# Kernel optimization log

Measured on AMD Instinct MI355X. Metric: run time of the kernel, lower is better.

## Reference

```python
import jax, jax.numpy as jnp
import numpy as np

D = 256          # config.entity_dim
DQ = 256         # query feature dim
G = 512          # number of neighbor groups (len(num_neighbors))
PER = 128
N = G * PER      # total candidate entities
CH = [256, 512, 512, 256]  # TCN channel list [D, 2D, 2D, D]
K = 3            # TCN kernel size
HID = 512        # policy net hidden dim


def _p(key, shape):
    return jax.random.normal(key, shape, dtype=jnp.float32) * 0.02


def setup_inputs() -> dict:
    key = jax.random.key(0)
    ks = jax.random.split(key, 32)
    inp = {}
    inp["NEs"] = jax.random.normal(ks[0], (N, D), dtype=jnp.float32)
    inp["nodes"] = jax.random.normal(ks[1], (G, D), dtype=jnp.float32)
    inp["query"] = jax.random.normal(ks[2], (G, DQ), dtype=jnp.float32)
    inp["num_neighbors"] = jnp.full((G,), PER, dtype=jnp.int32)
    inp["action_index"] = jax.random.randint(ks[3], (G,), 0, PER, dtype=jnp.int32)
    # action encoder (linear + relu)
    inp["Wa"] = _p(ks[4], (D, D))
    inp["ba"] = jnp.zeros((D,), jnp.float32)
    # TCN: 4 dilated causal conv levels, 1x1 downsample where channels change
    cin, i = D, 5
    for l, cout in enumerate(CH):
        inp[f"Wc{l}"] = _p(ks[i], (cout, cin, K)); i += 1
        inp[f"bc{l}"] = jnp.zeros((cout,), jnp.float32)
        if cout != cin:
            inp[f"Wd{l}"] = _p(ks[i], (cout, cin)); i += 1
        cin = cout
    # policy net MLP over [state_HS_per_candidate ; hat]
    inp["Wp1"] = _p(ks[i], (DQ + 2 * D + D, HID))
    inp["bp1"] = jnp.zeros((HID,), jnp.float32)
    inp["Wp2"] = _p(ks[i + 1], (HID, 1))
    inp["bp2"] = jnp.zeros((1,), jnp.float32)
    return inp


def _causal_conv(x, w, b, dil):
    # x: [1, C_in, L], w: [C_out, C_in, K] -> causal (left-padded) dilated conv
    k = w.shape[-1]
    y = jax.lax.conv_general_dilated(
        x, w, window_strides=(1,), padding=[((k - 1) * dil, 0)],
        rhs_dilation=(dil,), dimension_numbers=("NCH", "OIH", "NCH"))
    return y + b[None, :, None]


def _tcn(x, params):
    for (w, b, wd), dil in zip(params, (1, 2, 4, 8)):
        y = jax.nn.relu(_causal_conv(x, w, b, dil))
        res = x if wd is None else jnp.einsum("oi,bil->bol", wd, x)
        x = jax.nn.relu(y + res)
    return x


def reference(NEs, nodes, query, num_neighbors, action_index, Wa, ba,
              Wc0, bc0, Wc1, bc1, Wd1, Wc2, bc2, Wc3, bc3, Wd3,
              Wp1, bp1, Wp2, bp2):
    counts = np.asarray(num_neighbors)            # static ragged segment sizes
    g = counts.shape[0]
    seg = jnp.asarray(np.repeat(np.arange(g), counts))
    offsets = np.concatenate([[0], np.cumsum(counts)[:-1]])
    act = np.asarray(action_index)

    hats = jax.nn.relu(NEs @ Wa + ba)                         # [N, D]
    # _Max per group = column-wise max over each ragged segment
    HAts = jax.ops.segment_max(hats, seg, num_segments=g)     # [G, D]
    # chosen-action row per group (last group contributes no hat/node in the loop)
    hats_sel = hats[jnp.asarray(offsets[: g - 1] + act[: g - 1])]  # [G-1, D]

    # state_seq rows: (node_i, HAt_i, hat_i) for i < G-1, then nodes[-1]
    body = jnp.stack([nodes[: g - 1], HAts[: g - 1], hats_sel], axis=1)
    body = body.reshape(3 * (g - 1), -1)
    state_seq = jnp.concatenate([body, nodes[-1:]], axis=0)   # [L, D], L = 3(G-1)+1

    x = state_seq.T[None]                                     # [1, D, L]
    x = _tcn(x, [(Wc0, bc0, None), (Wc1, bc1, Wd1), (Wc2, bc2, None), (Wc3, bc3, Wd3)])
    hs = x[0].T[np.arange(g) * 3]                             # gather node positions -> [G, D]

    state_HS = jnp.concatenate([query, hs, HAts], axis=1)     # [G, DQ + 2D]
    rep = jnp.repeat(state_HS, jnp.asarray(counts), axis=0)   # [N, DQ + 2D]
    h = jax.nn.relu(jnp.concatenate([rep, hats], axis=1) @ Wp1 + bp1)
    Qsa = h @ Wp2 + bp2                                       # [N, 1]
    return Qsa
```

## Files before the change

kernel.cpp:

```cpp
#include <hip/hip_runtime.h>
#include <hip/hip_bf16.h>

#define D 256
#define G 512
#define PER 128
#define NROW (G*PER)
#define LSEQ 1534
#define LP 1536
#define HID 512

typedef __hip_bfloat16 bf16;
typedef __attribute__((ext_vector_type(8))) short bf16x8;
typedef __attribute__((ext_vector_type(4))) float f32x4;


__global__ __launch_bounds__(256) void k_prep(
    const float* __restrict__ Wa, bf16* __restrict__ WAhi, bf16* __restrict__ WAlo,
    const float* __restrict__ Wp1, bf16* __restrict__ WBt,
    bf16* __restrict__ WB1hi, bf16* __restrict__ WB1lo) {
  const int b = blockIdx.x, tid = threadIdx.x;
  if (b < 256) {
    int id = b * 256 + tid;
    int k = id >> 8, n = id & 255;
    float v = Wa[(size_t)k * D + n];
    bf16 h = __float2bfloat16(v);
    bf16 l = __float2bfloat16(v - __bfloat162float(h));
    int dst = (n >> 7) * 32768
            + (((((n >> 4) & 7) * 8 + (k >> 5)) * 64 + ((k >> 3) & 3) * 16 + (n & 15)) * 8)
            + (k & 7);
    WAhi[dst] = h;
    WAlo[dst] = l;
  } else if (b < 768) {
    int id = (b - 256) * 256 + tid;
    int k = id >> 9, n = id & 511;
    float v = Wp1[(size_t)(768 + k) * HID + n];
    int dst = (n >> 7) * 32768
            + (((((n >> 4) & 7) * 8 + (k >> 5)) * 64 + ((k >> 3) & 3) * 16 + (n & 15)) * 8)
            + (k & 7);
    WBt[dst] = __float2bfloat16(v);
  } else {
    int id = (b - 768) * 256 + tid;
    int k = id >> 9, n = id & 511;
    float v = Wp1[(size_t)k * HID + n];
    bf16 h = __float2bfloat16(v);
    bf16 l = __float2bfloat16(v - __bfloat162float(h));
    int kc = k >> 8, kr = k & 255;
    int nc = n >> 7, nr = n & 127;
    int dst = (nc*3 + kc) * 32768
            + ((((nr >> 4) * 8 + (kr >> 5)) * 64 + ((kr >> 3) & 3) * 16 + (nr & 15)) * 8)
            + (kr & 7);
    WB1hi[dst] = h;
    WB1lo[dst] = l;
  }
}

__global__ __launch_bounds__(256, 2) void k_hats_mfma(
    const float* __restrict__ NEs, const bf16* __restrict__ WAhi,
    const bf16* __restrict__ WAlo, const float* __restrict__ ba,
    bf16* __restrict__ hats, float* __restrict__ HAts) {
  __shared__ __align__(16) unsigned short bs[32768];
  __shared__ float wsmax[8][128];

  const int tid = threadIdx.x;
  const int wave = tid >> 6, lane = tid & 63;
  const int ln = lane & 15, quad = lane >> 4;
  const int row0 = blockIdx.x * 128;
  const int g = blockIdx.x;

  bf16x8 afH[2][8], afL[2][8];
  #pragma unroll
  for (int t = 0; t < 2; ++t) {
    const float4* ap = (const float4*)(NEs + (size_t)(row0 + (t*4 + wave)*16 + ln) * D);
    #pragma unroll
    for (int kt = 0; kt < 8; ++kt) {
      float4 x0 = ap[kt*8 + quad*2];
      float4 x1 = ap[kt*8 + quad*2 + 1];
      float xv[8] = {x0.x, x0.y, x0.z, x0.w, x1.x, x1.y, x1.z, x1.w};
      bf16x8 hv, lv;
      #pragma unroll
      for (int e = 0; e < 8; ++e) {
        bf16 h = __float2bfloat16(xv[e]);
        bf16 l = __float2bfloat16(xv[e] - __bfloat162float(h));
        hv[e] = *(short*)&h;
        lv[e] = *(short*)&l;
      }
      afH[t][kt] = hv;
      afL[t][kt] = lv;
    }
  }

  float* bsf = (float*)bs;

  for (int chunk = 0; chunk < 2; ++chunk) {
    f32x4 acc[2][8];
    #pragma unroll
    for (int t = 0; t < 2; ++t)
      #pragma unroll
      for (int nt = 0; nt < 8; ++nt) acc[t][nt] = (f32x4){0.f, 0.f, 0.f, 0.f};

    __syncthreads();
    {
      const uint4* src = (const uint4*)(WAhi + (size_t)chunk * 32768);
      uint4* dst = (uint4*)bs;
      #pragma unroll
      for (int r = 0; r < 16; ++r) dst[r*256 + tid] = src[r*256 + tid];
    }
    __syncthreads();
    #pragma unroll
    for (int nt = 0; nt < 8; ++nt)
      #pragma unroll
      for (int kt = 0; kt < 8; ++kt) {
        const bf16x8 bfr = *(const bf16x8*)&bs[((nt*8 + kt)*64 + lane)*8];
        acc[0][nt] = __builtin_amdgcn_mfma_f32_16x16x32_bf16(afH[0][kt], bfr, acc[0][nt], 0, 0, 0);
        acc[1][nt] = __builtin_amdgcn_mfma_f32_16x16x32_bf16(afH[1][kt], bfr, acc[1][nt], 0, 0, 0);
        acc[0][nt] = __builtin_amdgcn_mfma_f32_16x16x32_bf16(afL[0][kt], bfr, acc[0][nt], 0, 0, 0);
        acc[1][nt] = __builtin_amdgcn_mfma_f32_16x16x32_bf16(afL[1][kt], bfr, acc[1][nt], 0, 0, 0);
      }

    __syncthreads();
    {
      const uint4* src = (const uint4*)(WAlo + (size_t)chunk * 32768);
      uint4* dst = (uint4*)bs;
      #pragma unroll
      for (int r = 0; r < 16; ++r) dst[r*256 + tid] = src[r*256 + tid];
    }
    __syncthreads();
    #pragma unroll
    for (int nt = 0; nt < 8; ++nt)
      #pragma unroll
      for (int kt = 0; kt < 8; ++kt) {
        const bf16x8 bfr = *(const bf16x8*)&bs[((nt*8 + kt)*64 + lane)*8];
        acc[0][nt] = __builtin_amdgcn_mfma_f32_16x16x32_bf16(afH[0][kt], bfr, acc[0][nt], 0, 0, 0);
        acc[1][nt] = __builtin_amdgcn_mfma_f32_16x16x32_bf16(afH[1][kt], bfr, acc[1][nt], 0, 0, 0);
      }

    #pragma unroll
    for (int t = 0; t < 2; ++t) {
      __syncthreads();
      #pragma unroll
      for (int nt = 0; nt < 8; ++nt) {
        const float bv = ba[chunk*128 + nt*16 + ln];
        float m = 0.f;
        #pragma unroll
        for (int reg = 0; reg < 4; ++reg) {
          float h = acc[t][nt][reg] + bv;
          h = h > 0.f ? h : 0.f;
          bsf[(wave*16 + quad*4 + reg)*140 + nt*16 + ln] = h;
          m = fmaxf(m, h);
        }
        m = fmaxf(m, __shfl_xor(m, 16, 64));
        m = fmaxf(m, __shfl_xor(m, 32, 64));
        if (quad == 0) wsmax[t*4 + wave][nt*16 + ln] = m;
      }
      __syncthreads();
      {
        const int row = tid >> 2, q4 = tid & 3;
        const float* rp = &bsf[row*140 + q4*32];
        bf16* gp = hats + (size_t)(row0 + t*64 + row) * D + chunk*128 + q4*32;
        #pragma unroll
        for (int s = 0; s < 4; ++s) {
          float4 v0 = *(const float4*)&rp[s*8];
          float4 v1 = *(const float4*)&rp[s*8 + 4];
          float vv[8] = {v0.x, v0.y, v0.z, v0.w, v1.x, v1.y, v1.z, v1.w};
          bf16x8 pk;
          #pragma unroll
          for (int e = 0; e < 8; ++e) {
            bf16 b = __float2bfloat16(vv[e]);
            pk[e] = *(short*)&b;
          }
          *(bf16x8*)(gp + s*8) = pk;
        }
      }
    }
    if (tid < 128) {
      float m = wsmax[0][tid];
      #pragma unroll
      for (int w = 1; w < 8; ++w) m = fmaxf(m, wsmax[w][tid]);
      HAts[(size_t)g*D + chunk*128 + tid] = m;
    }
  }
}

__global__ void k_sprep(const float* __restrict__ query,
                        const float* __restrict__ HAts,
                        const float* __restrict__ xfin,
                        bf16* __restrict__ Shi, bf16* __restrict__ Slo) {
  int m = blockIdx.x * 256 + threadIdx.x;
  int g = blockIdx.y;
  float v;
  if (m < 256)      v = query[(size_t)g*D + m];
  else if (m < 512) v = xfin[(size_t)(m - 256)*LP + 3*g];
  else              v = HAts[(size_t)g*D + (m - 512)];
  bf16 h = __float2bfloat16(v);
  bf16 l = __float2bfloat16(v - __bfloat162float(h));
  Shi[(size_t)g*768 + m] = h;
  Slo[(size_t)g*768 + m] = l;
}

__global__ __launch_bounds__(256) void k_gterm_mfma(
    const bf16* __restrict__ Shi, const bf16* __restrict__ Slo,
    const bf16* __restrict__ WB1hi, const bf16* __restrict__ WB1lo,
    const float* __restrict__ bp1, float* __restrict__ Gterm) {
  __shared__ __align__(16) unsigned short bs[32768];

  const int tid = threadIdx.x;
  const int wave = tid >> 6, lane = tid & 63;
  const int ln = lane & 15, quad = lane >> 4;
  const int nc = blockIdx.x;
  const int row0 = blockIdx.y * 64;

  f32x4 acc[8];
  #pragma unroll
  for (int nt = 0; nt < 8; ++nt) acc[nt] = (f32x4){0.f, 0.f, 0.f, 0.f};

  const uint4* ahp = (const uint4*)(Shi + (size_t)(row0 + wave*16 + ln) * 768);
  const uint4* alp = (const uint4*)(Slo + (size_t)(row0 + wave*16 + ln) * 768);

  for (int kc = 0; kc < 3; ++kc) {
    bf16x8 afH[8], afL[8];
    #pragma unroll
    for (int kt = 0; kt < 8; ++kt) {
      uint4 th = ahp[kc*32 + kt*4 + quad];
      uint4 tl = alp[kc*32 + kt*4 + quad];
      afH[kt] = *(const bf16x8*)&th;
      afL[kt] = *(const bf16x8*)&tl;
    }

    __syncthreads();
    {
      const uint4* src = (const uint4*)(WB1hi + (size_t)(nc*3 + kc) * 32768);
      uint4* dst = (uint4*)bs;
      #pragma unroll
      for (int r = 0; r < 16; ++r) dst[r*256 + tid] = src[r*256 + tid];
    }
    __syncthreads();
    #pragma unroll
    for (int nt = 0; nt < 8; ++nt)
      #pragma unroll
      for (int kt = 0; kt < 8; ++kt) {
        const bf16x8 bfr = *(const bf16x8*)&bs[((nt*8 + kt)*64 + lane)*8];
        acc[nt] = __builtin_amdgcn_mfma_f32_16x16x32_bf16(afH[kt], bfr, acc[nt], 0, 0, 0);
        acc[nt] = __builtin_amdgcn_mfma_f32_16x16x32_bf16(afL[kt], bfr, acc[nt], 0, 0, 0);
      }

    __syncthreads();
    {
      const uint4* src = (const uint4*)(WB1lo + (size_t)(nc*3 + kc) * 32768);
      uint4* dst = (uint4*)bs;
      #pragma unroll
      for (int r = 0; r < 16; ++r) dst[r*256 + tid] = src[r*256 + tid];
    }
    __syncthreads();
    #pragma unroll
    for (int nt = 0; nt < 8; ++nt)
      #pragma unroll
      for (int kt = 0; kt < 8; ++kt) {
        const bf16x8 bfr = *(const bf16x8*)&bs[((nt*8 + kt)*64 + lane)*8];
        acc[nt] = __builtin_amdgcn_mfma_f32_16x16x32_bf16(afH[kt], bfr, acc[nt], 0, 0, 0);
      }
  }

  #pragma unroll
  for (int nt = 0; nt < 8; ++nt) {
    const int col = nc*128 + nt*16 + ln;
    const float bv = bp1[col];
    #pragma unroll
    for (int reg = 0; reg < 4; ++reg)
      Gterm[(size_t)(row0 + wave*16 + quad*4 + reg) * HID + col] = acc[nt][reg] + bv;
  }
}

__global__ void k_build_x0(const float* __restrict__ nodes,
                           const float* __restrict__ HAts,
                           const bf16* __restrict__ hats,
                           const int* __restrict__ act,
                           float* __restrict__ x0) {
  int t = blockIdx.x * 256 + threadIdx.x;
  int c = blockIdx.y;
  if (t >= LSEQ) return;
  float v;
  if (t == LSEQ - 1) {
    v = nodes[(size_t)(G-1)*D + c];
  } else {
    int r = t / 3, m = t - 3*r;
    if (m == 0)      v = nodes[(size_t)r*D + c];
    else if (m == 1) v = HAts[(size_t)r*D + c];
    else             v = __bfloat162float(hats[(size_t)(r*PER + act[r])*D + c]);
  }
  x0[(size_t)c*LP + t] = v;
}

template<int DIL, int CPB, bool HASWD>
__global__ __launch_bounds__(256) void k_tcn4(
    const float* __restrict__ xin,
    const float* __restrict__ W,
    const float* __restrict__ Wd,
    float* __restrict__ ybuf,
    float* __restrict__ rbuf,
    int Cin) {
  __shared__ __align__(16) float xs[32][80];
  __shared__ __align__(16) float wst[3][32][68];
  __shared__ __align__(16) float wds[HASWD ? 32 : 1][HASWD ? 68 : 4];

  const int tid = threadIdx.x;
  const int tt = tid & 15;
  const int cc = tid >> 4;
  const int t0 = blockIdx.x * 64;
  const int o0 = blockIdx.y * 64;
  const int Cout = gridDim.y << 6;

  float acc[4][4], res[4][4];
  #pragma unroll
  for (int it = 0; it < 4; ++it)
    #pragma unroll
    for (int ic = 0; ic < 4; ++ic) { acc[it][ic] = 0.f; res[it][ic] = 0.f; }

  for (int c = 0; c < CPB; ++c) {
    const int i0 = (blockIdx.z * CPB + c) * 32;
    __syncthreads();
    for (int idx = tid; idx < 32*20; idx += 256) {
      int r = idx / 20, j4 = idx - r*20;
      int tp = t0 - 16 + j4*4;
      float4 v;
      if (tp >= 0) v = *(const float4*)&xin[(size_t)(i0 + r)*LP + tp];
      else         v = make_float4(0.f, 0.f, 0.f, 0.f);
      *(float4*)&xs[r][j4*4] = v;
    }
    for (int idx = tid; idx < 64*32; idx += 256) {
      int o = idx >> 5, i = idx & 31;
      const float* wp = &W[((size_t)(o0 + o)*Cin + i0 + i)*3];
      wst[0][i][o] = wp[0];
      wst[1][i][o] = wp[1];
      wst[2][i][o] = wp[2];
      if constexpr (HASWD) wds[i][o] = Wd[(size_t)(o0 + o)*Cin + i0 + i];
    }
    __syncthreads();

    const int base = 16 + tt*4;
    #pragma unroll 2
    for (int i = 0; i < 32; ++i) {
      float4 xv0, xv1, xv2;
      if constexpr (DIL == 1) {
        float4 A = *(const float4*)&xs[i][base - 4];
        float4 B = *(const float4*)&xs[i][base];
        xv0 = make_float4(A.z, A.w, B.x, B.y);
        xv1 = make_float4(A.w, B.x, B.y, B.z);
        xv2 = B;
      } else if constexpr (DIL == 2) {
        float4 A = *(const float4*)&xs[i][base - 4];
        float4 B = *(const float4*)&xs[i][base];
        xv0 = A;
        xv1 = make_float4(A.z, A.w, B.x, B.y);
        xv2 = B;
      } else {
        xv0 = *(const float4*)&xs[i][base - 2*DIL];
        xv1 = *(const float4*)&xs[i][base - DIL];
        xv2 = *(const float4*)&xs[i][base];
      }
      float4 w0 = *(const float4*)&wst[0][i][cc*4];
      float4 w1 = *(const float4*)&wst[1][i][cc*4];
      float4 w2 = *(const float4*)&wst[2][i][cc*4];
      #pragma unroll
      for (int it = 0; it < 4; ++it) {
        float x0 = ((const float*)&xv0)[it];
        float x1 = ((const float*)&xv1)[it];
        float x2 = ((const float*)&xv2)[it];
        #pragma unroll
        for (int ic = 0; ic < 4; ++ic) {
          float a = acc[it][ic];
          a = fmaf(x0, ((const float*)&w0)[ic], a);
          a = fmaf(x1, ((const float*)&w1)[ic], a);
          a = fmaf(x2, ((const float*)&w2)[ic], a);
          acc[it][ic] = a;
        }
      }
      if constexpr (HASWD) {
        float4 wd4 = *(const float4*)&wds[i][cc*4];
        #pragma unroll
        for (int it = 0; it < 4; ++it) {
          float x2 = ((const float*)&xv2)[it];
          #pragma unroll
          for (int ic = 0; ic < 4; ++ic)
            res[it][ic] = fmaf(x2, ((const float*)&wd4)[ic], res[it][ic]);
        }
      }
    }
  }

  const int t = t0 + tt*4;
  #pragma unroll
  for (int ic = 0; ic < 4; ++ic) {
    const int ch = o0 + cc*4 + ic;
    const size_t off = ((size_t)blockIdx.z * Cout + ch) * LP + t;
    float4 v = make_float4(acc[0][ic], acc[1][ic], acc[2][ic], acc[3][ic]);
    *(float4*)&ybuf[off] = v;
    if constexpr (HASWD) {
      float4 rv = make_float4(res[0][ic], res[1][ic], res[2][ic], res[3][ic]);
      *(float4*)&rbuf[off] = rv;
    }
  }
}

template<int NZ, bool HASWD>
__global__ __launch_bounds__(384) void k_tcn_red(
    const float* __restrict__ ybuf, const float* __restrict__ rbuf,
    const float* __restrict__ xin, const float* __restrict__ b,
    float* __restrict__ xout) {
  const int ch = blockIdx.x;
  const int Cout = gridDim.x;
  const int t = threadIdx.x * 4;
  const size_t stride = (size_t)Cout * LP;
  const size_t base = (size_t)ch * LP + t;

  float4 y = *(const float4*)&ybuf[base];
  #pragma unroll
  for (int z = 1; z < NZ; ++z) {
    float4 u = *(const float4*)&ybuf[base + z*stride];
    y.x += u.x; y.y += u.y; y.z += u.z; y.w += u.w;
  }
  const float bv = b[ch];
  y.x = fmaxf(y.x + bv, 0.f); y.y = fmaxf(y.y + bv, 0.f);
  y.z = fmaxf(y.z + bv, 0.f); y.w = fmaxf(y.w + bv, 0.f);

  float4 r;
  if constexpr (HASWD) {
    r = *(const float4*)&rbuf[base];
    #pragma unroll
    for (int z = 1; z < NZ; ++z) {
      float4 u = *(const float4*)&rbuf[base + z*stride];
      r.x += u.x; r.y += u.y; r.z += u.z; r.w += u.w;
    }
  } else {
    r = *(const float4*)&xin[base];
  }
  float4 v;
  v.x = fmaxf(y.x + r.x, 0.f); v.y = fmaxf(y.y + r.y, 0.f);
  v.z = fmaxf(y.z + r.z, 0.f); v.w = fmaxf(y.w + r.w, 0.f);
  *(float4*)&xout[base] = v;
}

__global__ __launch_bounds__(256, 2) void k_final_mfma(
    const bf16* __restrict__ hats, const bf16* __restrict__ WBt,
    const float* __restrict__ Gterm, const float* __restrict__ Wp2,
    const float* __restrict__ bp2, float* __restrict__ out) {
  __shared__ __align__(16) unsigned short bs[32768];
  __shared__ float gs[512];
  __shared__ float w2s[512];

  const int tid = threadIdx.x;
  const int wave = tid >> 6, lane = tid & 63;
  const int ln = lane & 15, quad = lane >> 4;
  const int row0 = blockIdx.x * 128;
  const int g = blockIdx.x;

  gs[tid]        = Gterm[(size_t)g*HID + tid];
  gs[tid + 256]  = Gterm[(size_t)g*HID + tid + 256];
  w2s[tid]       = Wp2[tid];
  w2s[tid + 256] = Wp2[tid + 256];

  bf16x8 afrag[2][8];
  #pragma unroll
  for (int t = 0; t < 2; ++t) {
    const uint4* ap = (const uint4*)(hats + (size_t)(row0 + (t*4 + wave)*16 + ln) * D);
    #pragma unroll
    for (int kt = 0; kt < 8; ++kt) {
      uint4 u = ap[kt*4 + quad];
      afrag[t][kt] = *(const bf16x8*)&u;
    }
  }

  float osum[2][4] = {{0.f,0.f,0.f,0.f},{0.f,0.f,0.f,0.f}};

  for (int chunk = 0; chunk < 4; ++chunk) {
    __syncthreads();
    const uint4* src = (const uint4*)(WBt + (size_t)chunk * 32768);
    uint4* dst = (uint4*)bs;
    #pragma unroll
    for (int r = 0; r < 16; ++r) dst[r*256 + tid] = src[r*256 + tid];
    __syncthreads();

    #pragma unroll
    for (int nt = 0; nt < 8; ++nt) {
      f32x4 acc0 = {0.f, 0.f, 0.f, 0.f};
      f32x4 acc1 = {0.f, 0.f, 0.f, 0.f};
      #pragma unroll
      for (int kt = 0; kt < 8; ++kt) {
        const bf16x8 bfr = *(const bf16x8*)&bs[((nt*8 + kt)*64 + lane)*8];
        acc0 = __builtin_amdgcn_mfma_f32_16x16x32_bf16(afrag[0][kt], bfr, acc0, 0, 0, 0);
        acc1 = __builtin_amdgcn_mfma_f32_16x16x32_bf16(afrag[1][kt], bfr, acc1, 0, 0, 0);
      }
      int n = chunk*128 + nt*16 + ln;
      float gv = gs[n], wv = w2s[n];
      #pragma unroll
      for (int reg = 0; reg < 4; ++reg) {
        float h0 = acc0[reg] + gv;
        h0 = h0 > 0.f ? h0 : 0.f;
        osum[0][reg] = fmaf(h0, wv, osum[0][reg]);
        float h1 = acc1[reg] + gv;
        h1 = h1 > 0.f ? h1 : 0.f;
        osum[1][reg] = fmaf(h1, wv, osum[1][reg]);
      }
    }
  }

  #pragma unroll
  for (int t = 0; t < 2; ++t)
    #pragma unroll
    for (int reg = 0; reg < 4; ++reg) {
      float v = osum[t][reg];
      v += __shfl_xor(v, 1, 64);
      v += __shfl_xor(v, 2, 64);
      v += __shfl_xor(v, 4, 64);
      v += __shfl_xor(v, 8, 64);
      osum[t][reg] = v;
    }
  if (ln == 0) {
    float b2 = bp2[0];
    #pragma unroll
    for (int t = 0; t < 2; ++t)
      #pragma unroll
      for (int reg = 0; reg < 4; ++reg)
        out[row0 + (t*4 + wave)*16 + quad*4 + reg] = osum[t][reg] + b2;
  }
}

extern "C" void kernel_launch(void* const* d_in, const int* in_sizes, int n_in,
                              void* d_out, int out_size, void* d_ws, size_t ws_size,
                              hipStream_t stream) {
  (void)in_sizes; (void)n_in; (void)out_size; (void)ws_size;
  const float* NEs   = (const float*)d_in[0];
  const float* nodes = (const float*)d_in[1];
  const float* query = (const float*)d_in[2];
  const int*   act   = (const int*)d_in[4];
  const float* Wa    = (const float*)d_in[5];
  const float* ba    = (const float*)d_in[6];
  const float* Wc0   = (const float*)d_in[7];
  const float* bc0   = (const float*)d_in[8];
  const float* Wc1   = (const float*)d_in[9];
  const float* bc1   = (const float*)d_in[10];
  const float* Wd1   = (const float*)d_in[11];
  const float* Wc2   = (const float*)d_in[12];
  const float* bc2   = (const float*)d_in[13];
  const float* Wc3   = (const float*)d_in[14];
  const float* bc3   = (const float*)d_in[15];
  const float* Wd3   = (const float*)d_in[16];
  const float* Wp1   = (const float*)d_in[17];
  const float* bp1   = (const float*)d_in[18];
  const float* Wp2   = (const float*)d_in[19];
  const float* bp2   = (const float*)d_in[20];
  float* out = (float*)d_out;

  char* ws = (char*)d_ws;
  bf16*  hats  = (bf16*)ws;  ws += (size_t)NROW * D * sizeof(bf16);
  float* HAts  = (float*)ws; ws += (size_t)G * D * sizeof(float);
  float* xa    = (float*)ws; ws += (size_t)512 * LP * sizeof(float);
  float* xb    = (float*)ws; ws += (size_t)512 * LP * sizeof(float);
  float* Gterm = (float*)ws; ws += (size_t)G * HID * sizeof(float);
  bf16*  WBt   = (bf16*)ws;  ws += (size_t)D * HID * sizeof(bf16);
  bf16*  WAhi  = (bf16*)ws;  ws += (size_t)D * D * sizeof(bf16);
  bf16*  WAlo  = (bf16*)ws;  ws += (size_t)D * D * sizeof(bf16);
  bf16*  WB1hi = (bf16*)ws;  ws += (size_t)768 * HID * sizeof(bf16);
  bf16*  WB1lo = (bf16*)ws;  ws += (size_t)768 * HID * sizeof(bf16);
  bf16*  Shi   = (bf16*)ws;  ws += (size_t)G * 768 * sizeof(bf16);
  bf16*  Slo   = (bf16*)ws;  ws += (size_t)G * 768 * sizeof(bf16);
  float* P0 = (float*)ws; ws += (size_t)2048 * LP * sizeof(float);
  float* P1 = (float*)ws; ws += (size_t)2048 * LP * sizeof(float);

  k_prep<<<2304, 256, 0, stream>>>(Wa, WAhi, WAlo, Wp1, WBt, WB1hi, WB1lo);
  k_hats_mfma<<<G, 256, 0, stream>>>(NEs, WAhi, WAlo, ba, hats, HAts);
  k_build_x0<<<dim3(6, 256), 256, 0, stream>>>(nodes, HAts, hats, act, xa);

  k_tcn4<1, 1, false><<<dim3(24, 4, 8), 256, 0, stream>>>(xa, Wc0, nullptr, P0, nullptr, 256);
  k_tcn_red<8, false><<<256, 384, 0, stream>>>(P0, nullptr, xa, bc0, xb);
  k_tcn4<2, 2, true ><<<dim3(24, 8, 4), 256, 0, stream>>>(xb, Wc1, Wd1, P0, P1, 256);
  k_tcn_red<4, true ><<<512, 384, 0, stream>>>(P0, P1, xb, bc1, xa);
  k_tcn4<4, 4, false><<<dim3(24, 8, 4), 256, 0, stream>>>(xa, Wc2, nullptr, P0, nullptr, 512);
  k_tcn_red<4, false><<<512, 384, 0, stream>>>(P0, nullptr, xa, bc2, xb);
  k_tcn4<8, 2, true ><<<dim3(24, 4, 8), 256, 0, stream>>>(xb, Wc3, Wd3, P0, P1, 512);
  k_tcn_red<8, true ><<<256, 384, 0, stream>>>(P0, P1, xb, bc3, xa);

  k_sprep<<<dim3(3, G), 256, 0, stream>>>(query, HAts, xa, Shi, Slo);
  k_gterm_mfma<<<dim3(4, 8), 256, 0, stream>>>(Shi, Slo, WB1hi, WB1lo, bp1, Gterm);
  k_final_mfma<<<G, 256, 0, stream>>>(hats, WBt, Gterm, Wp2, bp2, out);
}
```

Measured before the change: 354.4 us.

## Process two groups per 512-thread block and swap MFMA operands for direct epilogue

The hats and final MFMA kernels now use 512-thread blocks that each cover two groups (256 rows), so every weight tile staged in LDS is reused by twice as many rows and the grid is halved. The MFMA operand order is swapped so each lane's accumulator holds four consecutive output columns of one row. This lets the hats epilogue store bf16 directly to global memory and reduce the column max with shuffles, dropping the LDS transpose staging and its extra barriers. The final kernel uses the same layout to cut the cross-lane reduction down to two shuffles. The cost is fewer, larger blocks (256 per kernel), and the previous two-blocks-per-CU occupancy hint is removed.

```diff
diff --git a/kernel.cpp b/kernel.cpp
--- a/kernel.cpp
+++ b/kernel.cpp
@@ -11,6 +11,7 @@
 
 typedef __hip_bfloat16 bf16;
 typedef __attribute__((ext_vector_type(8))) short bf16x8;
+typedef __attribute__((ext_vector_type(4))) short bf16x4;
 typedef __attribute__((ext_vector_type(4))) float f32x4;
 
 
@@ -54,7 +55,7 @@
   }
 }
 
-__global__ __launch_bounds__(256, 2) void k_hats_mfma(
+__global__ __launch_bounds__(512) void k_hats_mfma(
     const float* __restrict__ NEs, const bf16* __restrict__ WAhi,
     const bf16* __restrict__ WAlo, const float* __restrict__ ba,
     bf16* __restrict__ hats, float* __restrict__ HAts) {
@@ -64,13 +65,12 @@
   const int tid = threadIdx.x;
   const int wave = tid >> 6, lane = tid & 63;
   const int ln = lane & 15, quad = lane >> 4;
-  const int row0 = blockIdx.x * 128;
-  const int g = blockIdx.x;
+  const int row0 = blockIdx.x * 256;
 
   bf16x8 afH[2][8], afL[2][8];
   #pragma unroll
   for (int t = 0; t < 2; ++t) {
-    const float4* ap = (const float4*)(NEs + (size_t)(row0 + (t*4 + wave)*16 + ln) * D);
+    const float4* ap = (const float4*)(NEs + (size_t)(row0 + (wave*2 + t)*16 + ln) * D);
     #pragma unroll
     for (int kt = 0; kt < 8; ++kt) {
       float4 x0 = ap[kt*8 + quad*2];
@@ -89,8 +89,6 @@
     }
   }
 
-  float* bsf = (float*)bs;
-
   for (int chunk = 0; chunk < 2; ++chunk) {
     f32x4 acc[2][8];
     #pragma unroll
@@ -103,18 +101,18 @@
       const uint4* src = (const uint4*)(WAhi + (size_t)chunk * 32768);
       uint4* dst = (uint4*)bs;
       #pragma unroll
-      for (int r = 0; r < 16; ++r) dst[r*256 + tid] = src[r*256 + tid];
+      for (int r = 0; r < 8; ++r) dst[r*512 + tid] = src[r*512 + tid];
     }
     __syncthreads();
     #pragma unroll
     for (int nt = 0; nt < 8; ++nt)
       #pragma unroll
       for (int kt = 0; kt < 8; ++kt) {
-        const bf16x8 bfr = *(const bf16x8*)&bs[((nt*8 + kt)*64 + lane)*8];
-        acc[0][nt] = __builtin_amdgcn_mfma_f32_16x16x32_bf16(afH[0][kt], bfr, acc[0][nt], 0, 0, 0);
-        acc[1][nt] = __builtin_amdgcn_mfma_f32_16x16x32_bf16(afH[1][kt], bfr, acc[1][nt], 0, 0, 0);
-        acc[0][nt] = __builtin_amdgcn_mfma_f32_16x16x32_bf16(afL[0][kt], bfr, acc[0][nt], 0, 0, 0);
-        acc[1][nt] = __builtin_amdgcn_mfma_f32_16x16x32_bf16(afL[1][kt], bfr, acc[1][nt], 0, 0, 0);
+        const bf16x8 wfr = *(const bf16x8*)&bs[((nt*8 + kt)*64 + lane)*8];
+        acc[0][nt] = __builtin_amdgcn_mfma_f32_16x16x32_bf16(wfr, afH[0][kt], acc[0][nt], 0, 0, 0);
+        acc[1][nt] = __builtin_amdgcn_mfma_f32_16x16x32_bf16(wfr, afH[1][kt], acc[1][nt], 0, 0, 0);
+        acc[0][nt] = __builtin_amdgcn_mfma_f32_16x16x32_bf16(wfr, afL[0][kt], acc[0][nt], 0, 0, 0);
+        acc[1][nt] = __builtin_amdgcn_mfma_f32_16x16x32_bf16(wfr, afL[1][kt], acc[1][nt], 0, 0, 0);
       }
 
     __syncthreads();
@@ -122,61 +120,59 @@
       const uint4* src = (const uint4*)(WAlo + (size_t)chunk * 32768);
       uint4* dst = (uint4*)bs;
       #pragma unroll
-      for (int r = 0; r < 16; ++r) dst[r*256 + tid] = src[r*256 + tid];
+      for (int r = 0; r < 8; ++r) dst[r*512 + tid] = src[r*512 + tid];
     }
     __syncthreads();
     #pragma unroll
     for (int nt = 0; nt < 8; ++nt)
       #pragma unroll
       for (int kt = 0; kt < 8; ++kt) {
-        const bf16x8 bfr = *(const bf16x8*)&bs[((nt*8 + kt)*64 + lane)*8];
-        acc[0][nt] = __builtin_amdgcn_mfma_f32_16x16x32_bf16(afH[0][kt], bfr, acc[0][nt], 0, 0, 0);
-        acc[1][nt] = __builtin_amdgcn_mfma_f32_16x16x32_bf16(afH[1][kt], bfr, acc[1][nt], 0, 0, 0);
-      }
-
-    #pragma unroll
-    for (int t = 0; t < 2; ++t) {
-      __syncthreads();
-      #pragma unroll
-      for (int nt = 0; nt < 8; ++nt) {
-        const float bv = ba[chunk*128 + nt*16 + ln];
-        float m = 0.f;
+        const bf16x8 wfr = *(const bf16x8*)&bs[((nt*8 + kt)*64 + lane)*8];
+        acc[0][nt] = __builtin_amdgcn_mfma_f32_16x16x32_bf16(wfr, afH[0][kt], acc[0][nt], 0, 0, 0);
+        acc[1][nt] = __builtin_amdgcn_mfma_f32_16x16x32_bf16(wfr, afH[1][kt], acc[1][nt], 0, 0, 0);
+      }
+
+    #pragma unroll
+    for (int nt = 0; nt < 8; ++nt) {
+      const float4 bv = *(const float4*)&ba[chunk*128 + nt*16 + quad*4];
+      float m[4];
+      #pragma unroll
+      for (int t = 0; t < 2; ++t) {
+        bf16x4 pk;
         #pragma unroll
-        for (int reg = 0; reg < 4; ++reg) {
-          float h = acc[t][nt][reg] + bv;
+        for (int r = 0; r < 4; ++r) {
+          float h = acc[t][nt][r] + ((const float*)&bv)[r];
           h = h > 0.f ? h : 0.f;
-          bsf[(wave*16 + quad*4 + reg)*140 + nt*16 + ln] = h;
-          m = fmaxf(m, h);
+          bf16 hb = __float2bfloat16(h);
+          pk[r] = *(short*)&hb;
+          m[r] = (t == 0) ? h : fmaxf(m[r], h);
         }
-        m = fmaxf(m, __shfl_xor(m, 16, 64));
-        m = fmaxf(m, __shfl_xor(m, 32, 64));
-        if (quad == 0) wsmax[t*4 + wave][nt*16 + ln] = m;
-      }
-      __syncthreads();
-      {
-        const int row = tid >> 2, q4 = tid & 3;
-        const float* rp = &bsf[row*140 + q4*32];
-        bf16* gp = hats + (size_t)(row0 + t*64 + row) * D + chunk*128 + q4*32;
+        bf16* gp = hats + (size_t)(row0 + (wave*2 + t)*16 + ln) * D
+                 + chunk*128 + nt*16 + quad*4;
+        *(bf16x4*)gp = pk;
+      }
+      #pragma unroll
+      for (int r = 0; r < 4; ++r) {
+        m[r] = fmaxf(m[r], __shfl_xor(m[r], 1, 64));
+        m[r] = fmaxf(m[r], __shfl_xor(m[r], 2, 64));
+        m[r] = fmaxf(m[r], __shfl_xor(m[r], 4, 64));
+        m[r] = fmaxf(m[r], __shfl_xor(m[r], 8, 64));
+      }
+      if (ln == 0) {
         #pragma unroll
-        for (int s = 0; s < 4; ++s) {
-          float4 v0 = *(const float4*)&rp[s*8];
-          float4 v1 = *(const float4*)&rp[s*8 + 4];
-          float vv[8] = {v0.x, v0.y, v0.z, v0.w, v1.x, v1.y, v1.z, v1.w};
-          bf16x8 pk;
-          #pragma unroll
-          for (int e = 0; e < 8; ++e) {
-            bf16 b = __float2bfloat16(vv[e]);
-            pk[e] = *(short*)&b;
-          }
-          *(bf16x8*)(gp + s*8) = pk;
-        }
-      }
-    }
+        for (int r = 0; r < 4; ++r) wsmax[wave][nt*16 + quad*4 + r] = m[r];
+      }
+    }
+    __syncthreads();
     if (tid < 128) {
-      float m = wsmax[0][tid];
-      #pragma unroll
-      for (int w = 1; w < 8; ++w) m = fmaxf(m, wsmax[w][tid]);
-      HAts[(size_t)g*D + chunk*128 + tid] = m;
+      float m = fmaxf(fmaxf(wsmax[0][tid], wsmax[1][tid]),
+                      fmaxf(wsmax[2][tid], wsmax[3][tid]));
+      HAts[(size_t)(2*blockIdx.x)*D + chunk*128 + tid] = m;
+    } else if (tid < 256) {
+      int c = tid - 128;
+      float m = fmaxf(fmaxf(wsmax[4][c], wsmax[5][c]),
+                      fmaxf(wsmax[6][c], wsmax[7][c]));
+      HAts[(size_t)(2*blockIdx.x + 1)*D + chunk*128 + c] = m;
     }
   }
 }
@@ -439,44 +435,45 @@
   *(float4*)&xout[base] = v;
 }
 
-__global__ __launch_bounds__(256, 2) void k_final_mfma(
+__global__ __launch_bounds__(512) void k_final_mfma(
     const bf16* __restrict__ hats, const bf16* __restrict__ WBt,
     const float* __restrict__ Gterm, const float* __restrict__ Wp2,
     const float* __restrict__ bp2, float* __restrict__ out) {
   __shared__ __align__(16) unsigned short bs[32768];
-  __shared__ float gs[512];
-  __shared__ float w2s[512];
+  __shared__ __align__(16) float gs[2][512];
+  __shared__ __align__(16) float w2s[512];
 
   const int tid = threadIdx.x;
   const int wave = tid >> 6, lane = tid & 63;
   const int ln = lane & 15, quad = lane >> 4;
-  const int row0 = blockIdx.x * 128;
-  const int g = blockIdx.x;
-
-  gs[tid]        = Gterm[(size_t)g*HID + tid];
-  gs[tid + 256]  = Gterm[(size_t)g*HID + tid + 256];
-  w2s[tid]       = Wp2[tid];
-  w2s[tid + 256] = Wp2[tid + 256];
-
-  bf16x8 afrag[2][8];
+  const int row0 = blockIdx.x * 256;
+  const int gw = wave >> 2;
+
+  gs[0][tid & 511] = Gterm[(size_t)(2*blockIdx.x)*HID + tid];
+  gs[1][tid & 511] = Gterm[(size_t)(2*blockIdx.x + 1)*HID + tid];
+  if (tid < 512) w2s[tid] = Wp2[tid];
+
+  bf16x8 af[2][8];
   #pragma unroll
   for (int t = 0; t < 2; ++t) {
-    const uint4* ap = (const uint4*)(hats + (size_t)(row0 + (t*4 + wave)*16 + ln) * D);
+    const uint4* ap = (const uint4*)(hats + (size_t)(row0 + (wave*2 + t)*16 + ln) * D);
     #pragma unroll
     for (int kt = 0; kt < 8; ++kt) {
       uint4 u = ap[kt*4 + quad];
-      afrag[t][kt] = *(const bf16x8*)&u;
-    }
-  }
-
-  float osum[2][4] = {{0.f,0.f,0.f,0.f},{0.f,0.f,0.f,0.f}};
+      af[t][kt] = *(const bf16x8*)&u;
+    }
+  }
+
+  float osum[2] = {0.f, 0.f};
 
   for (int chunk = 0; chunk < 4; ++chunk) {
     __syncthreads();
-    const uint4* src = (const uint4*)(WBt + (size_t)chunk * 32768);
-    uint4* dst = (uint4*)bs;
-    #pragma unroll
-    for (int r = 0; r < 16; ++r) dst[r*256 + tid] = src[r*256 + tid];
+    {
+      const uint4* src = (const uint4*)(WBt + (size_t)chunk * 32768);
+      uint4* dst = (uint4*)bs;
+      #pragma unroll
+      for (int r = 0; r < 8; ++r) dst[r*512 + tid] = src[r*512 + tid];
+    }
     __syncthreads();
 
     #pragma unroll
@@ -485,42 +482,35 @@
       f32x4 acc1 = {0.f, 0.f, 0.f, 0.f};
       #pragma unroll
       for (int kt = 0; kt < 8; ++kt) {
-        const bf16x8 bfr = *(const bf16x8*)&bs[((nt*8 + kt)*64 + lane)*8];
-        acc0 = __builtin_amdgcn_mfma_f32_16x16x32_bf16(afrag[0][kt], bfr, acc0, 0, 0, 0);
-        acc1 = __builtin_amdgcn_mfma_f32_16x16x32_bf16(afrag[1][kt], bfr, acc1, 0, 0, 0);
-      }
-      int n = chunk*128 + nt*16 + ln;
-      float gv = gs[n], wv = w2s[n];
-      #pragma unroll
-      for (int reg = 0; reg < 4; ++reg) {
-        float h0 = acc0[reg] + gv;
+        const bf16x8 wfr = *(const bf16x8*)&bs[((nt*8 + kt)*64 + lane)*8];
+        acc0 = __builtin_amdgcn_mfma_f32_16x16x32_bf16(wfr, af[0][kt], acc0, 0, 0, 0);
+        acc1 = __builtin_amdgcn_mfma_f32_16x16x32_bf16(wfr, af[1][kt], acc1, 0, 0, 0);
+      }
+      const int n4 = chunk*128 + nt*16 + quad*4;
+      const float4 gv = *(const float4*)&gs[gw][n4];
+      const float4 wv = *(const float4*)&w2s[n4];
+      #pragma unroll
+      for (int r = 0; r < 4; ++r) {
+        float h0 = acc0[r] + ((const float*)&gv)[r];
         h0 = h0 > 0.f ? h0 : 0.f;
-        osum[0][reg] = fmaf(h0, wv, osum[0][reg]);
-        float h1 = acc1[reg] + gv;
+        osum[0] = fmaf(h0, ((const float*)&wv)[r], osum[0]);
+        float h1 = acc1[r] + ((const float*)&gv)[r];
         h1 = h1 > 0.f ? h1 : 0.f;
-        osum[1][reg] = fmaf(h1, wv, osum[1][reg]);
-      }
-    }
-  }
-
-  #pragma unroll
-  for (int t = 0; t < 2; ++t)
-    #pragma unroll
-    for (int reg = 0; reg < 4; ++reg) {
-      float v = osum[t][reg];
-      v += __shfl_xor(v, 1, 64);
-      v += __shfl_xor(v, 2, 64);
-      v += __shfl_xor(v, 4, 64);
-      v += __shfl_xor(v, 8, 64);
-      osum[t][reg] = v;
-    }
-  if (ln == 0) {
+        osum[1] = fmaf(h1, ((const float*)&wv)[r], osum[1]);
+      }
+    }
+  }
+
+  #pragma unroll
+  for (int t = 0; t < 2; ++t) {
+    osum[t] += __shfl_xor(osum[t], 16, 64);
+    osum[t] += __shfl_xor(osum[t], 32, 64);
+  }
+  if (quad == 0) {
     float b2 = bp2[0];
     #pragma unroll
     for (int t = 0; t < 2; ++t)
-      #pragma unroll
-      for (int reg = 0; reg < 4; ++reg)
-        out[row0 + (t*4 + wave)*16 + quad*4 + reg] = osum[t][reg] + b2;
+      out[row0 + (wave*2 + t)*16 + ln] = osum[t] + b2;
   }
 }
 
@@ -567,7 +557,7 @@
   float* P1 = (float*)ws; ws += (size_t)2048 * LP * sizeof(float);
 
   k_prep<<<2304, 256, 0, stream>>>(Wa, WAhi, WAlo, Wp1, WBt, WB1hi, WB1lo);
-  k_hats_mfma<<<G, 256, 0, stream>>>(NEs, WAhi, WAlo, ba, hats, HAts);
+  k_hats_mfma<<<256, 512, 0, stream>>>(NEs, WAhi, WAlo, ba, hats, HAts);
   k_build_x0<<<dim3(6, 256), 256, 0, stream>>>(nodes, HAts, hats, act, xa);
 
   k_tcn4<1, 1, false><<<dim3(24, 4, 8), 256, 0, stream>>>(xa, Wc0, nullptr, P0, nullptr, 256);
@@ -581,5 +571,5 @@
 
   k_sprep<<<dim3(3, G), 256, 0, stream>>>(query, HAts, xa, Shi, Slo);
   k_gterm_mfma<<<dim3(4, 8), 256, 0, stream>>>(Shi, Slo, WB1hi, WB1lo, bp1, Gterm);
-  k_final_mfma<<<G, 256, 0, stream>>>(hats, WBt, Gterm, Wp2, bp2, out);
-}
+  k_final_mfma<<<256, 512, 0, stream>>>(hats, WBt, Gterm, Wp2, bp2, out);
+}
```

Result: no change. 353.4 us (-0.3%).
